# Kernel optimization log

Measured on AMD Instinct MI355X. Metric: run time of the kernel, lower is better.

## Reference

```python
import jax, jax.numpy as jnp
import numpy as np

# HUSM region -> channel mapping (19 channels, 4 disjoint regions)
REGIONS = [
    [0, 1, 5, 8, 9, 10, 14],    # frontal
    [2, 11, 17],                # central
    [3, 12, 18],                # parietal
    [4, 6, 7, 13, 15, 16],      # occipital
]
N_CHAN = 19
N_REG = 4
_region_id = np.empty(N_CHAN, dtype=np.int32)
for r, chans in enumerate(REGIONS):
    for c in chans:
        _region_id[c] = r
REGION_ID = jnp.array(_region_id)
REGION_COUNTS = jnp.array([len(r) for r in REGIONS], dtype=jnp.float32)

N_HEADS, D_K, D_V, D_MODEL, D_FF = 8, 32, 32, 256, 1024
EPS = 1e-5


def layernorm(x):
    # default nn.LayerNorm: gamma=1, beta=0 (layer re-created each forward)
    mu = jnp.mean(x, axis=-1, keepdims=True)
    var = jnp.var(x, axis=-1, keepdims=True)
    return (x - mu) * jax.lax.rsqrt(var + EPS)


def mha(q_in, k_in, v_in, wq, wk, wv, wo):
    # q_in: [B, S, D]
    B, S, _ = q_in.shape
    Q = jnp.einsum('bsd,dhk->bhsk', q_in, wq.reshape(D_MODEL, N_HEADS, D_K))
    K = jnp.einsum('bsd,dhk->bhsk', k_in, wk.reshape(D_MODEL, N_HEADS, D_K))
    V = jnp.einsum('bsd,dhv->bhsv', v_in, wv.reshape(D_MODEL, N_HEADS, D_V))
    scores = jnp.einsum('bhqk,bhsk->bhqs', Q, K) / jnp.sqrt(jnp.float32(D_K))
    attn = jax.nn.softmax(scores, axis=-1)
    ctx = jnp.einsum('bhqs,bhsv->bqhv', attn, V).reshape(B, S, N_HEADS * D_V)
    return layernorm(ctx @ wo + q_in)


def setup_inputs() -> dict:
    key = jax.random.key(0)
    ks = jax.random.split(key, 12)
    B = 4096
    sc = 1.0 / np.sqrt(D_MODEL)
    inp = {
        'x': jax.random.normal(ks[0], (B, N_CHAN, D_MODEL), dtype=jnp.float32),
        'rsa_wq': jax.random.normal(ks[1], (D_MODEL, D_MODEL), dtype=jnp.float32) * sc,
        'rsa_wk': jax.random.normal(ks[2], (D_MODEL, D_MODEL), dtype=jnp.float32) * sc,
        'rsa_wv': jax.random.normal(ks[3], (D_MODEL, D_MODEL), dtype=jnp.float32) * sc,
        'rsa_wo': jax.random.normal(ks[4], (D_MODEL, D_MODEL), dtype=jnp.float32) * sc,
        'lsa_wq': jax.random.normal(ks[5], (D_MODEL, D_MODEL), dtype=jnp.float32) * sc,
        'lsa_wk': jax.random.normal(ks[6], (D_MODEL, D_MODEL), dtype=jnp.float32) * sc,
        'lsa_wv': jax.random.normal(ks[7], (D_MODEL, D_MODEL), dtype=jnp.float32) * sc,
        'lsa_wo': jax.random.normal(ks[8], (D_MODEL, D_MODEL), dtype=jnp.float32) * sc,
        'ffn_w1': jax.random.normal(ks[9], (D_MODEL, D_FF), dtype=jnp.float32) * sc,
        'ffn_w2': jax.random.normal(ks[10], (D_FF, D_MODEL), dtype=jnp.float32) * (1.0 / np.sqrt(D_FF)),
    }
    return inp


def reference(x, rsa_wq, rsa_wk, rsa_wv, rsa_wo,
              lsa_wq, lsa_wk, lsa_wv, lsa_wo, ffn_w1, ffn_w2):
    # --- region gather + avgpool: mean of channels per region -> [B, 4, D]
    fe_sum = jax.ops.segment_sum(jnp.swapaxes(x, 0, 1), REGION_ID,
                                 num_segments=N_REG)          # [4, B, D]
    fe_region = jnp.swapaxes(fe_sum, 0, 1) / REGION_COUNTS[None, :, None]
    # --- tiny 4-token region self-attention
    refined = mha(fe_region, fe_region, fe_region,
                  rsa_wq, rsa_wk, rsa_wv, rsa_wo)             # [B, 4, D]
    # --- scatter-add refined region feature back to its channels
    x = x + refined[:, REGION_ID, :]                          # [B, 19, D]
    # --- full-channel MHA + FFN
    fused = mha(x, x, x, lsa_wq, lsa_wk, lsa_wv, lsa_wo)
    ffn = jax.nn.relu(fused @ ffn_w1) @ ffn_w2
    return layernorm(ffn + fused)
```

## Files before the change

kernel.cpp:

```cpp
#include <hip/hip_runtime.h>
#include <stdint.h>
#include <stddef.h>


#define DEVINL __device__ __forceinline__

typedef __attribute__((ext_vector_type(8))) short short8;
typedef __attribute__((ext_vector_type(4))) float floatx4;
typedef __attribute__((ext_vector_type(8))) unsigned short ushort8;
typedef __attribute__((ext_vector_type(4))) unsigned short ushort4v;

DEVINL float bf2f(unsigned short u){
  union { unsigned int i; float f; } x; x.i = ((unsigned int)u) << 16; return x.f;
}
DEVINL unsigned short f2bf(float f){
  union { float f; unsigned int i; } x; x.f = f;
  unsigned int r = x.i + 0x7fffu + ((x.i >> 16) & 1u);
  return (unsigned short)(r >> 16);
}

typedef __attribute__((address_space(1))) void gvoid_t;
typedef __attribute__((address_space(3))) void lvoid_t;
DEVINL void gload_lds16(const void* g, void* l){
  __builtin_amdgcn_global_load_lds((gvoid_t*)g, (lvoid_t*)l, 16, 0, 0);
}

__global__ __launch_bounds__(256) void wprep_all(
    const float* __restrict__ rq, const float* __restrict__ rk,
    const float* __restrict__ rv, const float* __restrict__ ro,
    const float* __restrict__ lq, const float* __restrict__ lk,
    const float* __restrict__ lv, const float* __restrict__ lo,
    const float* __restrict__ w1, const float* __restrict__ w2,
    unsigned short* __restrict__ wt)
{
  int idx = blockIdx.x * 256 + threadIdx.x;
  const float* W; unsigned short* D; int N, r;
  const int K = (idx < 786432) ? 256 : 1024;
  if (idx < 524288){
    int wsel = idx >> 16; r = idx & 65535; N = 256; D = wt + wsel * 65536;
    switch (wsel){
      case 0: W = rq; break; case 1: W = rk; break; case 2: W = rv; break; case 3: W = ro; break;
      case 4: W = lq; break; case 5: W = lk; break; case 6: W = lv; break; default: W = lo; break;
    }
  } else if (idx < 786432){
    r = idx - 524288; N = 1024; D = wt + 524288; W = w1;
  } else {
    r = idx - 786432; N = 256; D = wt + 786432; W = w2;
  }
  int k = r / N, n = r - k * N;
  D[(size_t)n * K + k] = f2bf(W[r]);
}

__global__ __launch_bounds__(256) void pool_kernel(const float* __restrict__ x,
                                                   unsigned short* __restrict__ fe)
{
  const int b = blockIdx.x, d = threadIdx.x;
  const float* xb = x + (size_t)b * 4864 + d;
  float s0 = xb[0*256]+xb[1*256]+xb[5*256]+xb[8*256]+xb[9*256]+xb[10*256]+xb[14*256];
  float s1 = xb[2*256]+xb[11*256]+xb[17*256];
  float s2 = xb[3*256]+xb[12*256]+xb[18*256];
  float s3 = xb[4*256]+xb[6*256]+xb[7*256]+xb[13*256]+xb[15*256]+xb[16*256];
  unsigned short* fb = fe + (size_t)b * 1024 + d;
  fb[0]   = f2bf(s0 * (1.f/7.f));
  fb[256] = f2bf(s1 * (1.f/3.f));
  fb[512] = f2bf(s2 * (1.f/3.f));
  fb[768] = f2bf(s3 * (1.f/6.f));
}

template<int RELU>
__global__ __launch_bounds__(256, 2)
void gemm_kernel(const unsigned short* __restrict__ A,
                 const unsigned short* __restrict__ Bt,
                 unsigned short* __restrict__ C, int M, int N, int K)
{
  __shared__ __align__(1024) unsigned short lds[2][2][8192];
  const int tid  = threadIdx.x;
  const int wave = tid >> 6, lane = tid & 63;
  const int wm = wave >> 1, wn = wave & 1;
  const int rowA0 = blockIdx.x * 128;
  const int rowB0 = blockIdx.y * 128;
  const int stg_row = lane >> 3;
  const int stg_kb  = (((lane & 7) ^ (lane >> 3)) << 4);

  floatx4 acc[4][4];
  #pragma unroll
  for (int i = 0; i < 4; ++i)
    #pragma unroll
    for (int j = 0; j < 4; ++j) acc[i][j] = (floatx4){0.f, 0.f, 0.f, 0.f};

  const int nk = K >> 6;
  int cur = 0;
  #pragma unroll
  for (int s = 0; s < 4; ++s){
    int chunk = wave * 4 + s;
    int r = chunk * 8 + stg_row;
    gload_lds16((const char*)(A  + (size_t)(rowA0 + r) * K) + stg_kb,
                (char*)(&lds[0][0][0]) + chunk * 1024);
    gload_lds16((const char*)(Bt + (size_t)(rowB0 + r) * K) + stg_kb,
                (char*)(&lds[0][1][0]) + chunk * 1024);
  }
  __syncthreads();

  for (int kt = 0; kt < nk; ++kt){
    if (kt + 1 < nk){
      const int kbase = (kt + 1) << 7;
      #pragma unroll
      for (int s = 0; s < 4; ++s){
        int chunk = wave * 4 + s;
        int r = chunk * 8 + stg_row;
        gload_lds16((const char*)(A  + (size_t)(rowA0 + r) * K) + kbase + stg_kb,
                    (char*)(&lds[cur ^ 1][0][0]) + chunk * 1024);
        gload_lds16((const char*)(Bt + (size_t)(rowB0 + r) * K) + kbase + stg_kb,
                    (char*)(&lds[cur ^ 1][1][0]) + chunk * 1024);
      }
    }
    const char* As = (const char*)(&lds[cur][0][0]);
    const char* Bs = (const char*)(&lds[cur][1][0]);
    #pragma unroll
    for (int kk = 0; kk < 2; ++kk){
      short8 a[4], b[4];
      #pragma unroll
      for (int i = 0; i < 4; ++i){
        int row = wm * 64 + i * 16 + (lane & 15);
        int kb  = (kk * 64 + ((lane >> 4) << 4)) ^ ((row & 7) << 4);
        a[i] = *(const short8*)(As + row * 128 + kb);
      }
      #pragma unroll
      for (int j = 0; j < 4; ++j){
        int row = wn * 64 + j * 16 + (lane & 15);
        int kb  = (kk * 64 + ((lane >> 4) << 4)) ^ ((row & 7) << 4);
        b[j] = *(const short8*)(Bs + row * 128 + kb);
      }
      #pragma unroll
      for (int i = 0; i < 4; ++i)
        #pragma unroll
        for (int j = 0; j < 4; ++j)
          acc[i][j] = __builtin_amdgcn_mfma_f32_16x16x32_bf16(a[i], b[j], acc[i][j], 0, 0, 0);
    }
    __syncthreads();
    cur ^= 1;
  }

  const int cr = (lane >> 4) << 2;
  const int cc = lane & 15;
  #pragma unroll
  for (int i = 0; i < 4; ++i){
    #pragma unroll
    for (int j = 0; j < 4; ++j){
      int r0 = rowA0 + wm * 64 + i * 16 + cr;
      int c0 = rowB0 + wn * 64 + j * 16 + cc;
      #pragma unroll
      for (int r = 0; r < 4; ++r){
        float v = acc[i][j][r];
        if (RELU) v = fmaxf(v, 0.f);
        C[(size_t)(r0 + r) * N + c0] = f2bf(v);
      }
    }
  }
}

template<int OUTF32>
__global__ __launch_bounds__(512, 4)
void gemm_ln_kernel(const unsigned short* __restrict__ A,
                    const unsigned short* __restrict__ Bt,
                    const unsigned short* __restrict__ Res,
                    void* __restrict__ Out, int M, int K)
{
  __shared__ __align__(1024) char lds[2][40960];
  const int tid  = threadIdx.x;
  const int wave = tid >> 6, lane = tid & 63;
  const int wm = wave >> 2, wn = wave & 3;
  const int rowA0 = blockIdx.x * 64;
  const int stg_row = lane >> 3;
  const int stg_kb  = (((lane & 7) ^ (lane >> 3)) << 4);

  floatx4 acc[2][4];
  #pragma unroll
  for (int i = 0; i < 2; ++i)
    #pragma unroll
    for (int j = 0; j < 4; ++j) acc[i][j] = (floatx4){0.f, 0.f, 0.f, 0.f};

  const int nk = K >> 6;
  int cur = 0;
  #pragma unroll
  for (int s = 0; s < 5; ++s){
    int chunk = wave * 5 + s;
    const unsigned short* src = (chunk < 8)
      ? A  + (size_t)(rowA0 + chunk * 8 + stg_row) * K
      : Bt + (size_t)((chunk - 8) * 8 + stg_row) * K;
    gload_lds16((const char*)src + stg_kb, &lds[0][0] + chunk * 1024);
  }
  __syncthreads();

  for (int kt = 0; kt < nk; ++kt){
    if (kt + 1 < nk){
      const int kbase = (kt + 1) << 7;
      #pragma unroll
      for (int s = 0; s < 5; ++s){
        int chunk = wave * 5 + s;
        const unsigned short* src = (chunk < 8)
          ? A  + (size_t)(rowA0 + chunk * 8 + stg_row) * K
          : Bt + (size_t)((chunk - 8) * 8 + stg_row) * K;
        gload_lds16((const char*)src + kbase + stg_kb, &lds[cur ^ 1][0] + chunk * 1024);
      }
    }
    const char* As = &lds[cur][0];
    const char* Bs = &lds[cur][0] + 8192;
    #pragma unroll
    for (int kk = 0; kk < 2; ++kk){
      short8 a[2], b[4];
      #pragma unroll
      for (int i = 0; i < 2; ++i){
        int row = wm * 32 + i * 16 + (lane & 15);
        int kb  = (kk * 64 + ((lane >> 4) << 4)) ^ ((row & 7) << 4);
        a[i] = *(const short8*)(As + row * 128 + kb);
      }
      #pragma unroll
      for (int j = 0; j < 4; ++j){
        int row = wn * 64 + j * 16 + (lane & 15);
        int kb  = (kk * 64 + ((lane >> 4) << 4)) ^ ((row & 7) << 4);
        b[j] = *(const short8*)(Bs + row * 128 + kb);
      }
      #pragma unroll
      for (int i = 0; i < 2; ++i)
        #pragma unroll
        for (int j = 0; j < 4; ++j)
          acc[i][j] = __builtin_amdgcn_mfma_f32_16x16x32_bf16(a[i], b[j], acc[i][j], 0, 0, 0);
    }
    __syncthreads();
    cur ^= 1;
  }

  float* red_s = (float*)&lds[0][0];
  float* red_q = red_s + 256;
  float* mu_a  = red_s + 512;
  float* rs_a  = red_s + 576;
  const int g  = lane >> 4;
  const int cl = lane & 15;
  #pragma unroll
  for (int i = 0; i < 2; ++i){
    #pragma unroll
    for (int r = 0; r < 4; ++r){
      const int rowl = wm * 32 + i * 16 + g * 4 + r;
      float s = 0.f, q = 0.f;
      #pragma unroll
      for (int j = 0; j < 4; ++j){
        float v = acc[i][j][r] +
                  bf2f(Res[(size_t)(rowA0 + rowl) * 256 + wn * 64 + j * 16 + cl]);
        acc[i][j][r] = v;
        s += v; q += v * v;
      }
      #pragma unroll
      for (int off = 1; off < 16; off <<= 1){
        s += __shfl_xor(s, off); q += __shfl_xor(q, off);
      }
      if (cl == 0){ red_s[wn * 64 + rowl] = s; red_q[wn * 64 + rowl] = q; }
    }
  }
  __syncthreads();
  if (tid < 64){
    float S = red_s[tid] + red_s[64 + tid] + red_s[128 + tid] + red_s[192 + tid];
    float Q = red_q[tid] + red_q[64 + tid] + red_q[128 + tid] + red_q[192 + tid];
    float mu = S * (1.f / 256.f);
    float var = Q * (1.f / 256.f) - mu * mu;
    mu_a[tid] = mu;
    rs_a[tid] = rsqrtf(var + 1e-5f);
  }
  __syncthreads();
  #pragma unroll
  for (int i = 0; i < 2; ++i){
    #pragma unroll
    for (int r = 0; r < 4; ++r){
      const int rowl = wm * 32 + i * 16 + g * 4 + r;
      const float mu = mu_a[rowl], rs = rs_a[rowl];
      #pragma unroll
      for (int j = 0; j < 4; ++j){
        float w = (acc[i][j][r] - mu) * rs;
        size_t idx = (size_t)(rowA0 + rowl) * 256 + wn * 64 + j * 16 + cl;
        if (OUTF32) ((float*)Out)[idx] = w;
        else        ((unsigned short*)Out)[idx] = f2bf(w);
      }
    }
  }
}

__global__ __launch_bounds__(256) void attn4_kernel(
    const unsigned short* __restrict__ QKV, unsigned short* __restrict__ ctx)
{
  const int t = threadIdx.x;
  const int lb = t >> 5, u = t & 31, h = u >> 2, q = u & 3;
  const size_t b = (size_t)blockIdx.x * 8 + lb;
  const unsigned short* tb = QKV + b * 4 * 768;

  float qf[32];
  {
    const ushort8* qp = (const ushort8*)(tb + (size_t)q * 768 + h * 32);
    #pragma unroll
    for (int g = 0; g < 4; ++g){
      ushort8 v = qp[g];
      #pragma unroll
      for (int e = 0; e < 8; ++e) qf[g * 8 + e] = bf2f(v[e]);
    }
  }
  float sc[4];
  #pragma unroll
  for (int s = 0; s < 4; ++s){
    const ushort8* kp = (const ushort8*)(tb + (size_t)s * 768 + 256 + h * 32);
    float a0 = 0, a1 = 0, a2 = 0, a3 = 0;
    #pragma unroll
    for (int g = 0; g < 4; ++g){
      ushort8 v = kp[g];
      a0 += qf[g*8+0]*bf2f(v[0]); a1 += qf[g*8+1]*bf2f(v[1]);
      a2 += qf[g*8+2]*bf2f(v[2]); a3 += qf[g*8+3]*bf2f(v[3]);
      a0 += qf[g*8+4]*bf2f(v[4]); a1 += qf[g*8+5]*bf2f(v[5]);
      a2 += qf[g*8+6]*bf2f(v[6]); a3 += qf[g*8+7]*bf2f(v[7]);
    }
    sc[s] = ((a0 + a1) + (a2 + a3)) * 0.17677669529663687f;
  }
  float m = fmaxf(fmaxf(sc[0], sc[1]), fmaxf(sc[2], sc[3]));
  float sum = 0.f;
  #pragma unroll
  for (int s = 0; s < 4; ++s){ sc[s] = __expf(sc[s] - m); sum += sc[s]; }
  float inv = 1.f / sum;

  float o[32];
  #pragma unroll
  for (int d = 0; d < 32; ++d) o[d] = 0.f;
  #pragma unroll
  for (int s = 0; s < 4; ++s){
    float p = sc[s] * inv;
    const ushort8* vp = (const ushort8*)(tb + (size_t)s * 768 + 512 + h * 32);
    #pragma unroll
    for (int g = 0; g < 4; ++g){
      ushort8 v = vp[g];
      #pragma unroll
      for (int e = 0; e < 8; ++e) o[g * 8 + e] += p * bf2f(v[e]);
    }
  }
  unsigned short* cp = ctx + (b * 4 + q) * 256 + h * 32;
  #pragma unroll
  for (int g = 0; g < 4; ++g){
    ushort8 w;
    #pragma unroll
    for (int e = 0; e < 8; ++e) w[e] = f2bf(o[g * 8 + e]);
    ((ushort8*)cp)[g] = w;
  }
}

__global__ __launch_bounds__(256) void scatter_kernel(
    const float* __restrict__ x, const unsigned short* __restrict__ ref,
    unsigned short* __restrict__ x2)
{
  const int b = blockIdx.x, d = threadIdx.x;
  float rv[4];
  #pragma unroll
  for (int r = 0; r < 4; ++r) rv[r] = bf2f(ref[(size_t)b * 1024 + r * 256 + d]);
  const float* xb = x + (size_t)b * 4864 + d;
  unsigned short* xo = x2 + (size_t)b * 4864 + d;
  const int rid[19] = {0,0,1,2,3,0,3,3,0,0,0,1,2,3,0,3,3,1,2};
  #pragma unroll
  for (int c = 0; c < 19; ++c) xo[c * 256] = f2bf(xb[c * 256] + rv[rid[c]]);
}

__global__ __launch_bounds__(304) void attn19_kernel(
    const unsigned short* __restrict__ QKV, unsigned short* __restrict__ ctx)
{
  __shared__ float KV[38][320];
  const int tid = threadIdx.x;
  const size_t b = blockIdx.x;
  const unsigned short* base = QKV + b * 19 * 768;

  #pragma unroll
  for (int it = 0; it < 4; ++it){
    int c = tid + it * 304;
    int m = (c >= 608);
    int i = c - m * 608;
    int s = i >> 5, j = i & 31;
    ushort8 w = *(const ushort8*)(base + (size_t)s * 768 + 256 + (m << 8) + j * 8);
    int slot = j >> 1;
    int off = slot * 20 + (j & 1) * 8;
    float* dst = &KV[m * 19 + s][off];
    #pragma unroll
    for (int e = 0; e < 8; ++e) dst[e] = bf2f(w[e]);
  }
  __syncthreads();

  const int u = tid;
  const int q = u >> 4, h = (u >> 1) & 7, half = u & 1;
  const int slot = h * 2 + half;
  const int roff = slot * 20;

  float qf[16];
  {
    const ushort8* qp = (const ushort8*)(base + (size_t)q * 768 + h * 32 + half * 16);
    #pragma unroll
    for (int g = 0; g < 2; ++g){
      ushort8 v = qp[g];
      #pragma unroll
      for (int e = 0; e < 8; ++e) qf[g * 8 + e] = bf2f(v[e]);
    }
  }

  float p[19];
  float m = -1e30f;
  #pragma unroll
  for (int s = 0; s < 19; ++s){
    const float* kr = &KV[s][roff];
    float a0 = 0, a1 = 0, a2 = 0, a3 = 0;
    #pragma unroll
    for (int g = 0; g < 4; ++g){
      floatx4 kvv = *(const floatx4*)(kr + g * 4);
      a0 += qf[g*4+0] * kvv[0]; a1 += qf[g*4+1] * kvv[1];
      a2 += qf[g*4+2] * kvv[2]; a3 += qf[g*4+3] * kvv[3];
    }
    float part = (a0 + a1) + (a2 + a3);
    part += __shfl_xor(part, 1);
    p[s] = part * 0.17677669529663687f;
    m = fmaxf(m, p[s]);
  }
  float sum = 0.f;
  #pragma unroll
  for (int s = 0; s < 19; ++s){ p[s] = __expf(p[s] - m); sum += p[s]; }
  float inv = 1.f / sum;

  float o[16];
  #pragma unroll
  for (int d = 0; d < 16; ++d) o[d] = 0.f;
  #pragma unroll
  for (int s = 0; s < 19; ++s){
    float ps = p[s] * inv;
    const float* vr = &KV[19 + s][roff];
    #pragma unroll
    for (int g = 0; g < 4; ++g){
      floatx4 vv = *(const floatx4*)(vr + g * 4);
      o[g*4+0] += ps * vv[0]; o[g*4+1] += ps * vv[1];
      o[g*4+2] += ps * vv[2]; o[g*4+3] += ps * vv[3];
    }
  }
  unsigned short* cp = ctx + (b * 19 + q) * 256 + h * 32 + half * 16;
  #pragma unroll
  for (int g = 0; g < 2; ++g){
    ushort8 w;
    #pragma unroll
    for (int e = 0; e < 8; ++e) w[e] = f2bf(o[g * 8 + e]);
    ((ushort8*)cp)[g] = w;
  }
}

extern "C" void kernel_launch(void* const* d_in, const int* in_sizes, int n_in,
                              void* d_out, int out_size, void* d_ws, size_t ws_size,
                              hipStream_t stream)
{
  (void)n_in; (void)out_size;
  const float* x  = (const float*)d_in[0];
  const float* rq = (const float*)d_in[1];
  const float* rk = (const float*)d_in[2];
  const float* rv = (const float*)d_in[3];
  const float* ro = (const float*)d_in[4];
  const float* lq = (const float*)d_in[5];
  const float* lk = (const float*)d_in[6];
  const float* lv = (const float*)d_in[7];
  const float* lo = (const float*)d_in[8];
  const float* w1 = (const float*)d_in[9];
  const float* w2 = (const float*)d_in[10];

  const int B = in_sizes[0] / 4864;
  const int M4  = B * 4;
  const int M19 = B * 19;
  const int MH  = M19 / 2;
  const size_t MB = 1ull << 20;
  if (ws_size < 240 * MB) return;

  char* ws = (char*)d_ws;
  unsigned short* WT    = (unsigned short*)(ws);
  unsigned short* FE    = (unsigned short*)(ws + 2   * MB);
  unsigned short* QKV4  = (unsigned short*)(ws + 10  * MB);
  unsigned short* CTX4  = (unsigned short*)(ws + 34  * MB);
  unsigned short* REF   = (unsigned short*)(ws + 42  * MB);
  unsigned short* X2    = (unsigned short*)(ws + 50  * MB);
  unsigned short* QKV19 = (unsigned short*)(ws + 88  * MB);
  unsigned short* CTX19 = (unsigned short*)(ws + 202 * MB);
  unsigned short* FUSED = (unsigned short*)(ws + 88  * MB);
  unsigned short* H     = (unsigned short*)(ws + 126 * MB);
  float* out = (float*)d_out;

  wprep_all<<<4096, 256, 0, stream>>>(rq, rk, rv, ro, lq, lk, lv, lo, w1, w2, WT);
  pool_kernel<<<B, 256, 0, stream>>>(x, FE);
  gemm_kernel<0><<<dim3(M4/128, 6), 256, 0, stream>>>(FE, WT, QKV4, M4, 768, 256);
  attn4_kernel<<<B/8, 256, 0, stream>>>(QKV4, CTX4);
  gemm_ln_kernel<0><<<M4/64, 512, 0, stream>>>(CTX4, WT + 3*65536, FE, REF, M4, 256);
  scatter_kernel<<<B, 256, 0, stream>>>(x, REF, X2);
  gemm_kernel<0><<<dim3(M19/128, 6), 256, 0, stream>>>(X2, WT + 4*65536, QKV19, M19, 768, 256);
  attn19_kernel<<<B, 304, 0, stream>>>(QKV19, CTX19);
  gemm_ln_kernel<0><<<M19/64, 512, 0, stream>>>(CTX19, WT + 7*65536, X2, FUSED, M19, 256);
  for (int hf = 0; hf < 2; ++hf){
    const unsigned short* Fh = FUSED + (size_t)hf * MH * 256;
    gemm_kernel<1><<<dim3(MH/128, 8), 256, 0, stream>>>(Fh, WT + 524288, H, MH, 1024, 256);
    gemm_ln_kernel<1><<<MH/64, 512, 0, stream>>>(H, WT + 786432, Fh,
                                                 out + (size_t)hf * MH * 256, MH, 1024);
  }
}
```

Before: 415.2 us.

## Single-buffer GEMM LDS for higher occupancy and store attention K/V as bf16

The GEMM kernel drops LDS double buffering and moves to one 32KB tile buffer, raising the launch-bounds occupancy hint from 2 to 3 blocks per CU. Global-to-LDS loads are now issued and waited on at the start of each k-step, so the prefetch overlap is lost and the design relies on extra resident blocks to hide latency. The 19-token attention kernel keeps K/V in LDS as bf16 instead of fp32, halving its shared memory and converting to float at use. The half-size rows keep the padded stride, so LDS bank behaviour changes and conversion work moves into the inner loops.

```diff
diff --git a/kernel.cpp b/kernel.cpp
--- a/kernel.cpp
+++ b/kernel.cpp
@@ -68,12 +68,12 @@
 }
 
 template<int RELU>
-__global__ __launch_bounds__(256, 2)
+__global__ __launch_bounds__(256, 3)
 void gemm_kernel(const unsigned short* __restrict__ A,
                  const unsigned short* __restrict__ Bt,
                  unsigned short* __restrict__ C, int M, int N, int K)
 {
-  __shared__ __align__(1024) unsigned short lds[2][2][8192];
+  __shared__ __align__(1024) unsigned short lds[2][8192];
   const int tid  = threadIdx.x;
   const int wave = tid >> 6, lane = tid & 63;
   const int wm = wave >> 1, wn = wave & 1;
@@ -89,33 +89,21 @@
     for (int j = 0; j < 4; ++j) acc[i][j] = (floatx4){0.f, 0.f, 0.f, 0.f};
 
   const int nk = K >> 6;
-  int cur = 0;
-  #pragma unroll
-  for (int s = 0; s < 4; ++s){
-    int chunk = wave * 4 + s;
-    int r = chunk * 8 + stg_row;
-    gload_lds16((const char*)(A  + (size_t)(rowA0 + r) * K) + stg_kb,
-                (char*)(&lds[0][0][0]) + chunk * 1024);
-    gload_lds16((const char*)(Bt + (size_t)(rowB0 + r) * K) + stg_kb,
-                (char*)(&lds[0][1][0]) + chunk * 1024);
-  }
-  __syncthreads();
-
   for (int kt = 0; kt < nk; ++kt){
-    if (kt + 1 < nk){
-      const int kbase = (kt + 1) << 7;
-      #pragma unroll
-      for (int s = 0; s < 4; ++s){
-        int chunk = wave * 4 + s;
-        int r = chunk * 8 + stg_row;
-        gload_lds16((const char*)(A  + (size_t)(rowA0 + r) * K) + kbase + stg_kb,
-                    (char*)(&lds[cur ^ 1][0][0]) + chunk * 1024);
-        gload_lds16((const char*)(Bt + (size_t)(rowB0 + r) * K) + kbase + stg_kb,
-                    (char*)(&lds[cur ^ 1][1][0]) + chunk * 1024);
-      }
-    }
-    const char* As = (const char*)(&lds[cur][0][0]);
-    const char* Bs = (const char*)(&lds[cur][1][0]);
+    if (kt) __syncthreads();
+    const int kbase = kt << 7;
+    #pragma unroll
+    for (int s = 0; s < 4; ++s){
+      int chunk = wave * 4 + s;
+      int r = chunk * 8 + stg_row;
+      gload_lds16((const char*)(A  + (size_t)(rowA0 + r) * K) + kbase + stg_kb,
+                  (char*)(&lds[0][0]) + chunk * 1024);
+      gload_lds16((const char*)(Bt + (size_t)(rowB0 + r) * K) + kbase + stg_kb,
+                  (char*)(&lds[1][0]) + chunk * 1024);
+    }
+    __syncthreads();
+    const char* As = (const char*)(&lds[0][0]);
+    const char* Bs = (const char*)(&lds[1][0]);
     #pragma unroll
     for (int kk = 0; kk < 2; ++kk){
       short8 a[4], b[4];
@@ -137,8 +125,6 @@
         for (int j = 0; j < 4; ++j)
           acc[i][j] = __builtin_amdgcn_mfma_f32_16x16x32_bf16(a[i], b[j], acc[i][j], 0, 0, 0);
     }
-    __syncthreads();
-    cur ^= 1;
   }
 
   const int cr = (lane >> 4) << 2;
@@ -365,7 +351,7 @@
 __global__ __launch_bounds__(304) void attn19_kernel(
     const unsigned short* __restrict__ QKV, unsigned short* __restrict__ ctx)
 {
-  __shared__ float KV[38][320];
+  __shared__ unsigned short KV[38][320];
   const int tid = threadIdx.x;
   const size_t b = blockIdx.x;
   const unsigned short* base = QKV + b * 19 * 768;
@@ -378,10 +364,11 @@
     int s = i >> 5, j = i & 31;
     ushort8 w = *(const ushort8*)(base + (size_t)s * 768 + 256 + (m << 8) + j * 8);
     int slot = j >> 1;
-    int off = slot * 20 + (j & 1) * 8;
-    float* dst = &KV[m * 19 + s][off];
-    #pragma unroll
-    for (int e = 0; e < 8; ++e) dst[e] = bf2f(w[e]);
+    unsigned short* dst = &KV[m * 19 + s][slot * 20 + (j & 1) * 8];
+    ushort4v lo = {w[0], w[1], w[2], w[3]};
+    ushort4v hi = {w[4], w[5], w[6], w[7]};
+    *(ushort4v*)dst = lo;
+    *(ushort4v*)(dst + 4) = hi;
   }
   __syncthreads();
 
@@ -405,13 +392,13 @@
   float m = -1e30f;
   #pragma unroll
   for (int s = 0; s < 19; ++s){
-    const float* kr = &KV[s][roff];
+    const unsigned short* kr = &KV[s][roff];
     float a0 = 0, a1 = 0, a2 = 0, a3 = 0;
     #pragma unroll
     for (int g = 0; g < 4; ++g){
-      floatx4 kvv = *(const floatx4*)(kr + g * 4);
-      a0 += qf[g*4+0] * kvv[0]; a1 += qf[g*4+1] * kvv[1];
-      a2 += qf[g*4+2] * kvv[2]; a3 += qf[g*4+3] * kvv[3];
+      ushort4v kvv = *(const ushort4v*)(kr + g * 4);
+      a0 += qf[g*4+0] * bf2f(kvv[0]); a1 += qf[g*4+1] * bf2f(kvv[1]);
+      a2 += qf[g*4+2] * bf2f(kvv[2]); a3 += qf[g*4+3] * bf2f(kvv[3]);
     }
     float part = (a0 + a1) + (a2 + a3);
     part += __shfl_xor(part, 1);
@@ -429,12 +416,12 @@
   #pragma unroll
   for (int s = 0; s < 19; ++s){
     float ps = p[s] * inv;
-    const float* vr = &KV[19 + s][roff];
+    const unsigned short* vr = &KV[19 + s][roff];
     #pragma unroll
     for (int g = 0; g < 4; ++g){
-      floatx4 vv = *(const floatx4*)(vr + g * 4);
-      o[g*4+0] += ps * vv[0]; o[g*4+1] += ps * vv[1];
-      o[g*4+2] += ps * vv[2]; o[g*4+3] += ps * vv[3];
+      ushort4v vv = *(const ushort4v*)(vr + g * 4);
+      o[g*4+0] += ps * bf2f(vv[0]); o[g*4+1] += ps * bf2f(vv[1]);
+      o[g*4+2] += ps * bf2f(vv[2]); o[g*4+3] += ps * bf2f(vv[3]);
     }
   }
   unsigned short* cp = ctx + (b * 19 + q) * 256 + h * 32 + half * 16;
```

Result: no change. 416.3 us (+0.3%).
